# Kernel optimization log

Measured on AMD Instinct MI355X. Metric: run time of the kernel, lower is better.

## Reference

```python
import jax, jax.numpy as jnp
import numpy as np

B, IN, OUT, K = 2048, 1024, 1024, 20


def setup_inputs() -> dict:
    key = jax.random.key(0)
    k1, k2 = jax.random.split(key)
    x = jax.random.normal(k1, (B, IN), dtype=jnp.float32)
    # per-output, per-input spline coefficients: (out_features, in_features, num_knots)
    W = jax.random.normal(k2, (OUT, IN, K), dtype=jnp.float32) * 0.1
    # evenly spaced knot grid on [-2, 2] (linspace)
    knots = jnp.linspace(-2.0, 2.0, K, dtype=jnp.float32)
    return {"x": x, "W": W, "knots": knots}


def reference(x, W, knots):
    # RBF spline basis shared across all output features (this is the fusion
    # the original per-output Python loop misses):
    # basis[b, i, k] = exp(-0.5 * ((x[b, i] - knots[k]) / h)^2)
    h = knots[1] - knots[0]  # uniform knot spacing -> RBF bandwidth
    basis = jnp.exp(-0.5 * jnp.square((x[:, :, None] - knots) / h))  # (B, IN, K)
    # Each SplineLayer o computes sum_{i,k} W[o,i,k] * basis[b,i,k]; the
    # KANBlock concatenates the OUT scalars -> a single einsum.
    return jnp.einsum("bik,oik->bo", basis, W)  # (B, OUT)
```

## Files before the change

### kernel.cpp

```cpp
#include <hip/hip_runtime.h>

#define B_DIM 2048
#define IN_DIM 1024
#define OUT_DIM 1024
#define K_KNOTS 20
#define KR (IN_DIM * K_KNOTS)
#define OUT_ELEMS (B_DIM * OUT_DIM)

#define NB_QUADS (B_DIM * IN_DIM * 5)
#define NB_BASIS_BLK (NB_QUADS / 256)
#define NW4 (OUT_DIM * KR / 8)
#define NB_W_BLK (NW4 / 256)
#define NB_Z_BLK (OUT_ELEMS / (256 * 4))

typedef __bf16 bf16x8 __attribute__((ext_vector_type(8)));
typedef float  f32x4  __attribute__((ext_vector_type(4)));

#define MFMA16(a, b, c) __builtin_amdgcn_mfma_f32_16x16x32_bf16(a, b, c, 0, 0, 0)

__device__ __forceinline__ unsigned short f2bf(float f) {
    unsigned int u = __float_as_uint(f);
    unsigned int r = u + 0x7fffu + ((u >> 16) & 1u);
    return (unsigned short)(r >> 16);
}

__device__ __forceinline__ unsigned int pack2(float lo, float hi) {
    return (unsigned int)f2bf(lo) | ((unsigned int)f2bf(hi) << 16);
}

__device__ __forceinline__ void async_load16(const void* g, void* l) {
    __builtin_amdgcn_global_load_lds(
        (const __attribute__((address_space(1))) void*)g,
        (__attribute__((address_space(3))) void*)l,
        16, 0, 0);
}

__global__ void __launch_bounds__(256) prep_kernel(
        const float* __restrict__ x,
        const float4* __restrict__ Wsrc,
        const float* __restrict__ knots,
        uint2* __restrict__ basis_out,
        uint4* __restrict__ w_out,
        float* __restrict__ out) {
    if (blockIdx.x < NB_BASIS_BLK) {
        unsigned int n = blockIdx.x * 256 + threadIdx.x;
        unsigned int q  = n % 5u;
        unsigned int bi = n / 5u;
        float t0 = knots[0];
        float h  = knots[1] - t0;
        float invh = 1.0f / h;
        float xv = x[bi];
        float k0 = (float)(4 * q);
        float v[4];
#pragma unroll
        for (int j = 0; j < 4; ++j) {
            float t = __builtin_fmaf(k0 + (float)j, h, t0);
            float d = (xv - t) * invh;
            v[j] = __expf(-0.5f * d * d);
        }
        uint2 o;
        o.x = pack2(v[0], v[1]);
        o.y = pack2(v[2], v[3]);
        basis_out[n] = o;
    } else if (blockIdx.x < NB_BASIS_BLK + NB_W_BLK) {
        unsigned int t = (blockIdx.x - NB_BASIS_BLK) * 256 + threadIdx.x;
        float4 a = Wsrc[2 * t];
        float4 b = Wsrc[2 * t + 1];
        uint4 o;
        o.x = pack2(a.x, a.y);
        o.y = pack2(a.z, a.w);
        o.z = pack2(b.x, b.y);
        o.w = pack2(b.z, b.w);
        w_out[t] = o;
    } else {
        unsigned int t = (blockIdx.x - NB_BASIS_BLK - NB_W_BLK) * 256 + threadIdx.x;
        f32x4 z = {0.f, 0.f, 0.f, 0.f};
        *(f32x4*)(out + (size_t)t * 4) = z;
    }
}

#define AOFF(s, h) (((s) * 2 + (h)) * 8192)
#define BOFF(s, h) (32768 + ((s) * 2 + (h)) * 8192)

template <int S>
__device__ __forceinline__ void tile_step(
        int t, int ntiles,
        const unsigned short* __restrict__ Ab,
        const unsigned short* __restrict__ Bb,
        unsigned short* lds,
        f32x4 (&acc)[8][4],
        int m0, int n0, int k0,
        int wave, int wm, int wn, int r15, int c0, int c1,
        int srow8, int scol) {
    const int aB  = S * 16384 + (wm * 128 + r15) * 64;
    const int bB  = 32768 + S * 16384 + (wn * 64 + r15) * 64;
    const int kb1 = k0 + (t + 1) * 64;
    const bool st = (t + 1 < ntiles);

    auto stage = [&](const unsigned short* __restrict__ src, int grow, int kb, int lbase) {
        const unsigned short* g = src + (size_t)(grow + wave * 16 + srow8) * KR + kb + scol;
        async_load16(g,                  &lds[lbase + wave * 1024]);
        async_load16(g + (size_t)8 * KR, &lds[lbase + wave * 1024 + 512]);
    };

    bf16x8 a0[4], a1[4], b0[4], b1[4], s0[4], s1[4];

#pragma unroll
    for (int i = 0; i < 4; ++i) a0[i] = *(const bf16x8*)&lds[aB + i * 1024 + c0];
#pragma unroll
    for (int j = 0; j < 4; ++j) b0[j] = *(const bf16x8*)&lds[bB + j * 1024 + c0];
    __builtin_amdgcn_s_barrier();
    asm volatile("s_waitcnt lgkmcnt(0)" ::: "memory");
    __builtin_amdgcn_sched_barrier(0);
    __builtin_amdgcn_s_setprio(1);
#pragma unroll
    for (int i = 0; i < 4; ++i)
#pragma unroll
        for (int j = 0; j < 4; ++j)
            acc[i][j] = MFMA16(a0[i], b0[j], acc[i][j]);
    __builtin_amdgcn_s_setprio(0);

#pragma unroll
    for (int i = 0; i < 4; ++i) a1[i] = *(const bf16x8*)&lds[aB + i * 1024 + c1];
#pragma unroll
    for (int j = 0; j < 4; ++j) b1[j] = *(const bf16x8*)&lds[bB + j * 1024 + c1];
    __builtin_amdgcn_s_barrier();
    asm volatile("s_waitcnt lgkmcnt(0)" ::: "memory");
    __builtin_amdgcn_sched_barrier(0);
    __builtin_amdgcn_s_setprio(1);
#pragma unroll
    for (int i = 0; i < 4; ++i)
#pragma unroll
        for (int j = 0; j < 4; ++j)
            acc[i][j] = MFMA16(a1[i], b1[j], acc[i][j]);
    __builtin_amdgcn_s_setprio(0);

#pragma unroll
    for (int i = 0; i < 4; ++i) s0[i] = *(const bf16x8*)&lds[aB + (4 + i) * 1024 + c0];
    if (st) {
        stage(Ab, m0,       kb1, AOFF(S ^ 1, 0));
        stage(Ab, m0 + 128, kb1, AOFF(S ^ 1, 1));
    }
    __builtin_amdgcn_s_barrier();
    asm volatile("s_waitcnt lgkmcnt(0)" ::: "memory");
    __builtin_amdgcn_sched_barrier(0);
    __builtin_amdgcn_s_setprio(1);
#pragma unroll
    for (int i = 0; i < 4; ++i)
#pragma unroll
        for (int j = 0; j < 4; ++j)
            acc[4 + i][j] = MFMA16(s0[i], b0[j], acc[4 + i][j]);
    __builtin_amdgcn_s_setprio(0);

#pragma unroll
    for (int i = 0; i < 4; ++i) s1[i] = *(const bf16x8*)&lds[aB + (4 + i) * 1024 + c1];
    if (st) {
        stage(Bb, n0,       kb1, BOFF(S ^ 1, 0));
        stage(Bb, n0 + 128, kb1, BOFF(S ^ 1, 1));
    }
    __builtin_amdgcn_s_barrier();
    asm volatile("s_waitcnt lgkmcnt(0)" ::: "memory");
    __builtin_amdgcn_sched_barrier(0);
    __builtin_amdgcn_s_setprio(1);
#pragma unroll
    for (int i = 0; i < 4; ++i)
#pragma unroll
        for (int j = 0; j < 4; ++j)
            acc[4 + i][j] = MFMA16(s1[i], b1[j], acc[4 + i][j]);
    __builtin_amdgcn_s_setprio(0);

    if (st) asm volatile("s_waitcnt vmcnt(0)" ::: "memory");
    __builtin_amdgcn_s_barrier();
}

template <int KS, bool ATOMIC>
__device__ __forceinline__ void gemm_body(
        const unsigned short* __restrict__ Ab,
        const unsigned short* __restrict__ Bb,
        float* __restrict__ out,
        unsigned short* lds) {
    constexpr int KPBk   = KR / KS;
    constexpr int NTILES = KPBk / 64;

    const int id  = blockIdx.x;
    const int z   = id & 7;
    const int ord = id >> 3;
    const int mt  = ord & 7;
    const int nt  = ord >> 3;
    const int m0  = mt * 256;
    const int n0  = nt * 256;
    const int k0  = z * KPBk;

    const int tid  = threadIdx.x;
    const int wave = tid >> 6;
    const int lane = tid & 63;
    const int wm   = wave >> 2;
    const int wn   = wave & 3;

    const int srow8 = lane >> 3;
    const int scol  = ((lane & 7) ^ srow8) * 8;

    auto stage = [&](const unsigned short* __restrict__ src, int grow, int kb, int lbase) {
        const unsigned short* g = src + (size_t)(grow + wave * 16 + srow8) * KR + kb + scol;
        async_load16(g,                  &lds[lbase + wave * 1024]);
        async_load16(g + (size_t)8 * KR, &lds[lbase + wave * 1024 + 512]);
    };

    f32x4 acc[8][4];
#pragma unroll
    for (int i = 0; i < 8; ++i)
#pragma unroll
        for (int j = 0; j < 4; ++j) acc[i][j] = (f32x4){0.f, 0.f, 0.f, 0.f};

    const int q   = lane >> 4;
    const int r15 = lane & 15;
    const int r7  = lane & 7;
    const int c0  = (q ^ r7) * 8;
    const int c1  = ((4 + q) ^ r7) * 8;

    stage(Ab, m0,       k0, AOFF(0, 0));
    stage(Ab, m0 + 128, k0, AOFF(0, 1));
    stage(Bb, n0,       k0, BOFF(0, 0));
    stage(Bb, n0 + 128, k0, BOFF(0, 1));
    asm volatile("s_waitcnt vmcnt(0)" ::: "memory");
    __builtin_amdgcn_s_barrier();

    for (int tt = 0; tt < NTILES; tt += 2) {
        tile_step<0>(tt,     NTILES, Ab, Bb, lds, acc, m0, n0, k0,
                     wave, wm, wn, r15, c0, c1, srow8, scol);
        tile_step<1>(tt + 1, NTILES, Ab, Bb, lds, acc, m0, n0, k0,
                     wave, wm, wn, r15, c0, c1, srow8, scol);
    }

    float* dst = ATOMIC ? out : out + (size_t)z * OUT_ELEMS;
#pragma unroll
    for (int i = 0; i < 8; ++i)
#pragma unroll
        for (int j = 0; j < 4; ++j)
#pragma unroll
            for (int r = 0; r < 4; ++r) {
                const int row = m0 + wm * 128 + i * 16 + q * 4 + r;
                const int c   = n0 + wn * 64  + j * 16 + r15;
                if (ATOMIC)
                    atomicAdd(&dst[(size_t)row * OUT_DIM + c], acc[i][j][r]);
                else
                    dst[(size_t)row * OUT_DIM + c] = acc[i][j][r];
            }
}

template <int KS, bool ATOMIC>
__global__ void __launch_bounds__(512, 2)
kan_gemm8(const unsigned short* __restrict__ Ab,
          const unsigned short* __restrict__ Bb,
          float* __restrict__ out) {
    __shared__ __align__(16) unsigned short lds[65536];
    gemm_body<KS, ATOMIC>(Ab, Bb, out, lds);
}

template <int KS>
__global__ void kan_reduce(const float* __restrict__ part, float* __restrict__ out) {
    const int idx = (blockIdx.x * 256 + threadIdx.x) * 4;
    f32x4 s = *(const f32x4*)(part + idx);
#pragma unroll
    for (int z = 1; z < KS; ++z)
        s += *(const f32x4*)(part + (size_t)z * OUT_ELEMS + idx);
    *(f32x4*)(out + idx) = s;
}

__global__ void kan_fallback(const float* __restrict__ x,
                             const float* __restrict__ W,
                             const float* __restrict__ knots,
                             float* __restrict__ out) {
    __shared__ float basis[256 * K_KNOTS];
    const int b = blockIdx.x;
    const int o = blockIdx.y * blockDim.x + threadIdx.x;
    const float invh = 1.0f / (knots[1] - knots[0]);
    const float* w = W + (size_t)o * KR;
    float sum = 0.f;
    for (int i0 = 0; i0 < IN_DIM; i0 += 256) {
        __syncthreads();
        for (int idx = threadIdx.x; idx < 256 * K_KNOTS; idx += blockDim.x) {
            const int i = i0 + idx / K_KNOTS;
            const int k = idx % K_KNOTS;
            const float d = (x[(size_t)b * IN_DIM + i] - knots[k]) * invh;
            basis[idx] = __expf(-0.5f * d * d);
        }
        __syncthreads();
        for (int r = 0; r < 256 * K_KNOTS; ++r)
            sum += basis[r] * w[(size_t)i0 * K_KNOTS + r];
    }
    out[(size_t)b * OUT_DIM + o] = sum;
}

extern "C" void kernel_launch(void* const* d_in, const int* in_sizes, int n_in,
                              void* d_out, int out_size, void* d_ws, size_t ws_size,
                              hipStream_t stream) {
    const float* x     = (const float*)d_in[0];
    const float* W     = (const float*)d_in[1];
    const float* knots = (const float*)d_in[2];
    float* out = (float*)d_out;

    const size_t basis_bytes = (size_t)B_DIM * KR * 2;
    const size_t wb_bytes    = (size_t)OUT_DIM * KR * 2;
    const size_t part8_bytes = (size_t)8 * OUT_ELEMS * 4;

    unsigned short* Ab = (unsigned short*)d_ws;
    unsigned short* Bb = (unsigned short*)((char*)d_ws + basis_bytes);
    float* part = (float*)((char*)d_ws + basis_bytes + wb_bytes);

    if (ws_size >= basis_bytes + wb_bytes) {
        prep_kernel<<<dim3(NB_BASIS_BLK + NB_W_BLK + NB_Z_BLK), dim3(256), 0, stream>>>(
            x, (const float4*)W, knots, (uint2*)Ab, (uint4*)Bb, out);
        kan_gemm8<8, true><<<dim3(256), dim3(512), 0, stream>>>(Ab, Bb, out);
        (void)part; (void)part8_bytes;
    } else {
        kan_fallback<<<dim3(B_DIM, OUT_DIM / 256), dim3(256), 0, stream>>>(x, W, knots, out);
    }
}
```

Before: 273.9 us.

## Fuse basis generation and W bf16 conversion into GEMM tile staging

Removes the separate prep kernel that materialised the bf16 basis matrix and bf16 W copy in global memory. Each GEMM block now computes RBF basis values from x and converts fp32 W to bf16 on the fly, writing both into LDS through register stores instead of async global-to-LDS loads. Atomic accumulation is replaced with split-K partial buffers plus a separate reduce kernel. This trades the global round-trip of the intermediates for redundant exp computation (each basis tile is recomputed by every N-tile block), synchronous register-path loads that may expose latency, and extra traffic for the partial sums.

```diff
diff --git a/kernel.cpp b/kernel.cpp
--- a/kernel.cpp
+++ b/kernel.cpp
@@ -6,12 +6,7 @@
 #define K_KNOTS 20
 #define KR (IN_DIM * K_KNOTS)
 #define OUT_ELEMS (B_DIM * OUT_DIM)
-
-#define NB_QUADS (B_DIM * IN_DIM * 5)
-#define NB_BASIS_BLK (NB_QUADS / 256)
-#define NW4 (OUT_DIM * KR / 8)
-#define NB_W_BLK (NW4 / 256)
-#define NB_Z_BLK (OUT_ELEMS / (256 * 4))
+#define KS 8
 
 typedef __bf16 bf16x8 __attribute__((ext_vector_type(8)));
 typedef float  f32x4  __attribute__((ext_vector_type(4)));
@@ -28,80 +23,51 @@
     return (unsigned int)f2bf(lo) | ((unsigned int)f2bf(hi) << 16);
 }
 
-__device__ __forceinline__ void async_load16(const void* g, void* l) {
-    __builtin_amdgcn_global_load_lds(
-        (const __attribute__((address_space(1))) void*)g,
-        (__attribute__((address_space(3))) void*)l,
-        16, 0, 0);
-}
-
-__global__ void __launch_bounds__(256) prep_kernel(
-        const float* __restrict__ x,
-        const float4* __restrict__ Wsrc,
-        const float* __restrict__ knots,
-        uint2* __restrict__ basis_out,
-        uint4* __restrict__ w_out,
-        float* __restrict__ out) {
-    if (blockIdx.x < NB_BASIS_BLK) {
-        unsigned int n = blockIdx.x * 256 + threadIdx.x;
-        unsigned int q  = n % 5u;
-        unsigned int bi = n / 5u;
-        float t0 = knots[0];
-        float h  = knots[1] - t0;
-        float invh = 1.0f / h;
-        float xv = x[bi];
-        float k0 = (float)(4 * q);
-        float v[4];
-#pragma unroll
-        for (int j = 0; j < 4; ++j) {
-            float t = __builtin_fmaf(k0 + (float)j, h, t0);
-            float d = (xv - t) * invh;
-            v[j] = __expf(-0.5f * d * d);
-        }
-        uint2 o;
-        o.x = pack2(v[0], v[1]);
-        o.y = pack2(v[2], v[3]);
-        basis_out[n] = o;
-    } else if (blockIdx.x < NB_BASIS_BLK + NB_W_BLK) {
-        unsigned int t = (blockIdx.x - NB_BASIS_BLK) * 256 + threadIdx.x;
-        float4 a = Wsrc[2 * t];
-        float4 b = Wsrc[2 * t + 1];
-        uint4 o;
-        o.x = pack2(a.x, a.y);
-        o.y = pack2(a.z, a.w);
-        o.z = pack2(b.x, b.y);
-        o.w = pack2(b.z, b.w);
-        w_out[t] = o;
-    } else {
-        unsigned int t = (blockIdx.x - NB_BASIS_BLK - NB_W_BLK) * 256 + threadIdx.x;
-        f32x4 z = {0.f, 0.f, 0.f, 0.f};
-        *(f32x4*)(out + (size_t)t * 4) = z;
-    }
+__device__ __forceinline__ uint4 basis8(const float* __restrict__ x,
+                                        int row, int cb,
+                                        float t0k, float h, float invh) {
+    const int i0  = cb / K_KNOTS;
+    const int kk0 = cb - i0 * K_KNOTS;
+    const int i1  = i0 + (i0 < IN_DIM - 1 ? 1 : 0);
+    const float xv0 = x[(size_t)row * IN_DIM + i0];
+    const float xv1 = x[(size_t)row * IN_DIM + i1];
+    float v[8];
+#pragma unroll
+    for (int j = 0; j < 8; ++j) {
+        const int kk   = kk0 + j;
+        const bool cr  = kk >= K_KNOTS;
+        const float xv = cr ? xv1 : xv0;
+        const float kf = (float)(cr ? kk - K_KNOTS : kk);
+        const float tt = __builtin_fmaf(kf, h, t0k);
+        const float d  = (xv - tt) * invh;
+        v[j] = __expf(-0.5f * d * d);
+    }
+    uint4 o;
+    o.x = pack2(v[0], v[1]); o.y = pack2(v[2], v[3]);
+    o.z = pack2(v[4], v[5]); o.w = pack2(v[6], v[7]);
+    return o;
 }
 
 #define AOFF(s, h) (((s) * 2 + (h)) * 8192)
 #define BOFF(s, h) (32768 + ((s) * 2 + (h)) * 8192)
 
 template <int S>
-__device__ __forceinline__ void tile_step(
+__device__ __forceinline__ void tile_step_f(
         int t, int ntiles,
-        const unsigned short* __restrict__ Ab,
-        const unsigned short* __restrict__ Bb,
+        const float* __restrict__ x,
+        const float* __restrict__ Wf,
         unsigned short* lds,
         f32x4 (&acc)[8][4],
         int m0, int n0, int k0,
-        int wave, int wm, int wn, int r15, int c0, int c1,
-        int srow8, int scol) {
-    const int aB  = S * 16384 + (wm * 128 + r15) * 64;
-    const int bB  = 32768 + S * 16384 + (wn * 64 + r15) * 64;
-    const int kb1 = k0 + (t + 1) * 64;
-    const bool st = (t + 1 < ntiles);
-
-    auto stage = [&](const unsigned short* __restrict__ src, int grow, int kb, int lbase) {
-        const unsigned short* g = src + (size_t)(grow + wave * 16 + srow8) * KR + kb + scol;
-        async_load16(g,                  &lds[lbase + wave * 1024]);
-        async_load16(g + (size_t)8 * KR, &lds[lbase + wave * 1024 + 512]);
-    };
+        int wave, int lane, int wm, int wn, int r15, int c0, int c1,
+        int srow8, int scol,
+        float t0k, float h, float invh) {
+    const int aB   = S * 16384 + (wm * 128 + r15) * 64;
+    const int bB   = 32768 + S * 16384 + (wn * 64 + r15) * 64;
+    const int kb1  = k0 + (t + 1) * 64;
+    const bool st  = (t + 1 < ntiles);
+    const int cbn  = kb1 + scol;
+    const int ldsw = wave * 1024 + lane * 8;
 
     bf16x8 a0[4], a1[4], b0[4], b1[4], s0[4], s1[4];
 
@@ -137,10 +103,6 @@
 
 #pragma unroll
     for (int i = 0; i < 4; ++i) s0[i] = *(const bf16x8*)&lds[aB + (4 + i) * 1024 + c0];
-    if (st) {
-        stage(Ab, m0,       kb1, AOFF(S ^ 1, 0));
-        stage(Ab, m0 + 128, kb1, AOFF(S ^ 1, 1));
-    }
     __builtin_amdgcn_s_barrier();
     asm volatile("s_waitcnt lgkmcnt(0)" ::: "memory");
     __builtin_amdgcn_sched_barrier(0);
@@ -152,12 +114,29 @@
             acc[4 + i][j] = MFMA16(s0[i], b0[j], acc[4 + i][j]);
     __builtin_amdgcn_s_setprio(0);
 
+    f32x4 wA0, wA1, wB0, wB1, wC0, wC1, wD0, wD1;
+    if (st) {
+        const float* g0 = Wf + (size_t)(n0 + wave * 16 + srow8) * KR + cbn;
+        const float* g1 = g0 + (size_t)8 * KR;
+        const float* g2 = g0 + (size_t)128 * KR;
+        const float* g3 = g0 + (size_t)136 * KR;
+        wA0 = *(const f32x4*)g0;       wA1 = *(const f32x4*)(g0 + 4);
+        wB0 = *(const f32x4*)g1;       wB1 = *(const f32x4*)(g1 + 4);
+        wC0 = *(const f32x4*)g2;       wC1 = *(const f32x4*)(g2 + 4);
+        wD0 = *(const f32x4*)g3;       wD1 = *(const f32x4*)(g3 + 4);
+        const int ra = m0 + wave * 16 + srow8;
+        uint4 d0 = basis8(x, ra,       cbn, t0k, h, invh);
+        uint4 d1 = basis8(x, ra + 8,   cbn, t0k, h, invh);
+        uint4 d2 = basis8(x, ra + 128, cbn, t0k, h, invh);
+        uint4 d3 = basis8(x, ra + 136, cbn, t0k, h, invh);
+        *(uint4*)&lds[AOFF(S ^ 1, 0) + ldsw]       = d0;
+        *(uint4*)&lds[AOFF(S ^ 1, 0) + 512 + ldsw] = d1;
+        *(uint4*)&lds[AOFF(S ^ 1, 1) + ldsw]       = d2;
+        *(uint4*)&lds[AOFF(S ^ 1, 1) + 512 + ldsw] = d3;
+    }
+
 #pragma unroll
     for (int i = 0; i < 4; ++i) s1[i] = *(const bf16x8*)&lds[aB + (4 + i) * 1024 + c1];
-    if (st) {
-        stage(Bb, n0,       kb1, BOFF(S ^ 1, 0));
-        stage(Bb, n0 + 128, kb1, BOFF(S ^ 1, 1));
-    }
     __builtin_amdgcn_s_barrier();
     asm volatile("s_waitcnt lgkmcnt(0)" ::: "memory");
     __builtin_amdgcn_sched_barrier(0);
@@ -169,16 +148,32 @@
             acc[4 + i][j] = MFMA16(s1[i], b1[j], acc[4 + i][j]);
     __builtin_amdgcn_s_setprio(0);
 
-    if (st) asm volatile("s_waitcnt vmcnt(0)" ::: "memory");
-    __builtin_amdgcn_s_barrier();
-}
-
-template <int KS, bool ATOMIC>
-__device__ __forceinline__ void gemm_body(
-        const unsigned short* __restrict__ Ab,
-        const unsigned short* __restrict__ Bb,
-        float* __restrict__ out,
-        unsigned short* lds) {
+    if (st) {
+        uint4 o0 = make_uint4(pack2(wA0[0], wA0[1]), pack2(wA0[2], wA0[3]),
+                              pack2(wA1[0], wA1[1]), pack2(wA1[2], wA1[3]));
+        uint4 o1 = make_uint4(pack2(wB0[0], wB0[1]), pack2(wB0[2], wB0[3]),
+                              pack2(wB1[0], wB1[1]), pack2(wB1[2], wB1[3]));
+        uint4 o2 = make_uint4(pack2(wC0[0], wC0[1]), pack2(wC0[2], wC0[3]),
+                              pack2(wC1[0], wC1[1]), pack2(wC1[2], wC1[3]));
+        uint4 o3 = make_uint4(pack2(wD0[0], wD0[1]), pack2(wD0[2], wD0[3]),
+                              pack2(wD1[0], wD1[1]), pack2(wD1[2], wD1[3]));
+        *(uint4*)&lds[BOFF(S ^ 1, 0) + ldsw]       = o0;
+        *(uint4*)&lds[BOFF(S ^ 1, 0) + 512 + ldsw] = o1;
+        *(uint4*)&lds[BOFF(S ^ 1, 1) + ldsw]       = o2;
+        *(uint4*)&lds[BOFF(S ^ 1, 1) + 512 + ldsw] = o3;
+    }
+
+    asm volatile("s_waitcnt lgkmcnt(0)" ::: "memory");
+    __builtin_amdgcn_s_barrier();
+}
+
+__global__ void __launch_bounds__(512, 2)
+kan_gemmf(const float* __restrict__ x,
+          const float* __restrict__ Wf,
+          const float* __restrict__ knots,
+          float* __restrict__ part) {
+    __shared__ __align__(16) unsigned short lds[65536];
+
     constexpr int KPBk   = KR / KS;
     constexpr int NTILES = KPBk / 64;
 
@@ -200,11 +195,9 @@
     const int srow8 = lane >> 3;
     const int scol  = ((lane & 7) ^ srow8) * 8;
 
-    auto stage = [&](const unsigned short* __restrict__ src, int grow, int kb, int lbase) {
-        const unsigned short* g = src + (size_t)(grow + wave * 16 + srow8) * KR + kb + scol;
-        async_load16(g,                  &lds[lbase + wave * 1024]);
-        async_load16(g + (size_t)8 * KR, &lds[lbase + wave * 1024 + 512]);
-    };
+    const float t0k  = knots[0];
+    const float h    = knots[1] - t0k;
+    const float invh = 1.0f / h;
 
     f32x4 acc[8][4];
 #pragma unroll
@@ -218,21 +211,52 @@
     const int c0  = (q ^ r7) * 8;
     const int c1  = ((4 + q) ^ r7) * 8;
 
-    stage(Ab, m0,       k0, AOFF(0, 0));
-    stage(Ab, m0 + 128, k0, AOFF(0, 1));
-    stage(Bb, n0,       k0, BOFF(0, 0));
-    stage(Bb, n0 + 128, k0, BOFF(0, 1));
-    asm volatile("s_waitcnt vmcnt(0)" ::: "memory");
-    __builtin_amdgcn_s_barrier();
+    {
+        const int cb0  = k0 + scol;
+        const int ldsw = wave * 1024 + lane * 8;
+        const int ra   = m0 + wave * 16 + srow8;
+        uint4 d0 = basis8(x, ra,       cb0, t0k, h, invh);
+        uint4 d1 = basis8(x, ra + 8,   cb0, t0k, h, invh);
+        uint4 d2 = basis8(x, ra + 128, cb0, t0k, h, invh);
+        uint4 d3 = basis8(x, ra + 136, cb0, t0k, h, invh);
+        *(uint4*)&lds[AOFF(0, 0) + ldsw]       = d0;
+        *(uint4*)&lds[AOFF(0, 0) + 512 + ldsw] = d1;
+        *(uint4*)&lds[AOFF(0, 1) + ldsw]       = d2;
+        *(uint4*)&lds[AOFF(0, 1) + 512 + ldsw] = d3;
+        const float* g0 = Wf + (size_t)(n0 + wave * 16 + srow8) * KR + cb0;
+        const float* g1 = g0 + (size_t)8 * KR;
+        const float* g2 = g0 + (size_t)128 * KR;
+        const float* g3 = g0 + (size_t)136 * KR;
+        f32x4 wA0 = *(const f32x4*)g0, wA1 = *(const f32x4*)(g0 + 4);
+        f32x4 wB0 = *(const f32x4*)g1, wB1 = *(const f32x4*)(g1 + 4);
+        f32x4 wC0 = *(const f32x4*)g2, wC1 = *(const f32x4*)(g2 + 4);
+        f32x4 wD0 = *(const f32x4*)g3, wD1 = *(const f32x4*)(g3 + 4);
+        uint4 o0 = make_uint4(pack2(wA0[0], wA0[1]), pack2(wA0[2], wA0[3]),
+                              pack2(wA1[0], wA1[1]), pack2(wA1[2], wA1[3]));
+        uint4 o1 = make_uint4(pack2(wB0[0], wB0[1]), pack2(wB0[2], wB0[3]),
+                              pack2(wB1[0], wB1[1]), pack2(wB1[2], wB1[3]));
+        uint4 o2 = make_uint4(pack2(wC0[0], wC0[1]), pack2(wC0[2], wC0[3]),
+                              pack2(wC1[0], wC1[1]), pack2(wC1[2], wC1[3]));
+        uint4 o3 = make_uint4(pack2(wD0[0], wD0[1]), pack2(wD0[2], wD0[3]),
+                              pack2(wD1[0], wD1[1]), pack2(wD1[2], wD1[3]));
+        *(uint4*)&lds[BOFF(0, 0) + ldsw]       = o0;
+        *(uint4*)&lds[BOFF(0, 0) + 512 + ldsw] = o1;
+        *(uint4*)&lds[BOFF(0, 1) + ldsw]       = o2;
+        *(uint4*)&lds[BOFF(0, 1) + 512 + ldsw] = o3;
+        asm volatile("s_waitcnt lgkmcnt(0)" ::: "memory");
+        __builtin_amdgcn_s_barrier();
+    }
 
     for (int tt = 0; tt < NTILES; tt += 2) {
-        tile_step<0>(tt,     NTILES, Ab, Bb, lds, acc, m0, n0, k0,
-                     wave, wm, wn, r15, c0, c1, srow8, scol);
-        tile_step<1>(tt + 1, NTILES, Ab, Bb, lds, acc, m0, n0, k0,
-                     wave, wm, wn, r15, c0, c1, srow8, scol);
-    }
-
-    float* dst = ATOMIC ? out : out + (size_t)z * OUT_ELEMS;
+        tile_step_f<0>(tt,     NTILES, x, Wf, lds, acc, m0, n0, k0,
+                       wave, lane, wm, wn, r15, c0, c1, srow8, scol,
+                       t0k, h, invh);
+        tile_step_f<1>(tt + 1, NTILES, x, Wf, lds, acc, m0, n0, k0,
+                       wave, lane, wm, wn, r15, c0, c1, srow8, scol,
+                       t0k, h, invh);
+    }
+
+    float* dst = part + (size_t)z * OUT_ELEMS;
 #pragma unroll
     for (int i = 0; i < 8; ++i)
 #pragma unroll
@@ -241,28 +265,16 @@
             for (int r = 0; r < 4; ++r) {
                 const int row = m0 + wm * 128 + i * 16 + q * 4 + r;
                 const int c   = n0 + wn * 64  + j * 16 + r15;
-                if (ATOMIC)
-                    atomicAdd(&dst[(size_t)row * OUT_DIM + c], acc[i][j][r]);
-                else
-                    dst[(size_t)row * OUT_DIM + c] = acc[i][j][r];
+                dst[(size_t)row * OUT_DIM + c] = acc[i][j][r];
             }
 }
 
-template <int KS, bool ATOMIC>
-__global__ void __launch_bounds__(512, 2)
-kan_gemm8(const unsigned short* __restrict__ Ab,
-          const unsigned short* __restrict__ Bb,
-          float* __restrict__ out) {
-    __shared__ __align__(16) unsigned short lds[65536];
-    gemm_body<KS, ATOMIC>(Ab, Bb, out, lds);
-}
-
-template <int KS>
+template <int KSr>
 __global__ void kan_reduce(const float* __restrict__ part, float* __restrict__ out) {
     const int idx = (blockIdx.x * 256 + threadIdx.x) * 4;
     f32x4 s = *(const f32x4*)(part + idx);
 #pragma unroll
-    for (int z = 1; z < KS; ++z)
+    for (int z = 1; z < KSr; ++z)
         s += *(const f32x4*)(part + (size_t)z * OUT_ELEMS + idx);
     *(f32x4*)(out + idx) = s;
 }
@@ -300,19 +312,12 @@
     const float* knots = (const float*)d_in[2];
     float* out = (float*)d_out;
 
-    const size_t basis_bytes = (size_t)B_DIM * KR * 2;
-    const size_t wb_bytes    = (size_t)OUT_DIM * KR * 2;
-    const size_t part8_bytes = (size_t)8 * OUT_ELEMS * 4;
-
-    unsigned short* Ab = (unsigned short*)d_ws;
-    unsigned short* Bb = (unsigned short*)((char*)d_ws + basis_bytes);
-    float* part = (float*)((char*)d_ws + basis_bytes + wb_bytes);
-
-    if (ws_size >= basis_bytes + wb_bytes) {
-        prep_kernel<<<dim3(NB_BASIS_BLK + NB_W_BLK + NB_Z_BLK), dim3(256), 0, stream>>>(
-            x, (const float4*)W, knots, (uint2*)Ab, (uint4*)Bb, out);
-        kan_gemm8<8, true><<<dim3(256), dim3(512), 0, stream>>>(Ab, Bb, out);
-        (void)part; (void)part8_bytes;
+    const size_t part_bytes = (size_t)KS * OUT_ELEMS * 4;
+    float* part = (float*)d_ws;
+
+    if (ws_size >= part_bytes) {
+        kan_gemmf<<<dim3(256), dim3(512), 0, stream>>>(x, W, knots, part);
+        kan_reduce<KS><<<dim3(OUT_ELEMS / (256 * 4)), dim3(256), 0, stream>>>(part, out);
     } else {
         kan_fallback<<<dim3(B_DIM, OUT_DIM / 256), dim3(256), 0, stream>>>(x, W, knots, out);
     }
```

New measurement: 282.0 us. +3.0%, slower.

## Replace atomic split-K output with partial buffers plus reduce; widen basis stores

Applied to the files above, without the earlier changes.

The GEMM no longer zeroes the output and atomically adds its eight split-K partials. Each split now writes plain stores into its own partial buffer, and a separate reduce kernel sums the eight slices. The basis prep kernel also computes two quads per thread and writes 16-byte stores, handling the case where a pair spans two inputs. This removes atomic contention and the zeroing pass, but adds 64 MB of partial writes plus reads, one more kernel launch, and a larger workspace requirement.

```diff
diff --git a/kernel.cpp b/kernel.cpp
--- a/kernel.cpp
+++ b/kernel.cpp
@@ -6,12 +6,12 @@
 #define K_KNOTS 20
 #define KR (IN_DIM * K_KNOTS)
 #define OUT_ELEMS (B_DIM * OUT_DIM)
-
-#define NB_QUADS (B_DIM * IN_DIM * 5)
-#define NB_BASIS_BLK (NB_QUADS / 256)
+#define KS 8
+
+#define NPAIRS (B_DIM * IN_DIM * 5 / 2)
+#define NB_BASIS_BLK (NPAIRS / 256)
 #define NW4 (OUT_DIM * KR / 8)
 #define NB_W_BLK (NW4 / 256)
-#define NB_Z_BLK (OUT_ELEMS / (256 * 4))
 
 typedef __bf16 bf16x8 __attribute__((ext_vector_type(8)));
 typedef float  f32x4  __attribute__((ext_vector_type(4)));
@@ -39,30 +39,42 @@
         const float* __restrict__ x,
         const float4* __restrict__ Wsrc,
         const float* __restrict__ knots,
-        uint2* __restrict__ basis_out,
-        uint4* __restrict__ w_out,
-        float* __restrict__ out) {
+        uint4* __restrict__ basis_out,
+        uint4* __restrict__ w_out) {
     if (blockIdx.x < NB_BASIS_BLK) {
-        unsigned int n = blockIdx.x * 256 + threadIdx.x;
-        unsigned int q  = n % 5u;
-        unsigned int bi = n / 5u;
-        float t0 = knots[0];
-        float h  = knots[1] - t0;
-        float invh = 1.0f / h;
-        float xv = x[bi];
-        float k0 = (float)(4 * q);
-        float v[4];
+        const unsigned int p  = blockIdx.x * 256 + threadIdx.x;
+        const unsigned int n0 = 2 * p;
+        const unsigned int q0  = n0 % 5u;
+        const unsigned int bi0 = n0 / 5u;
+        const float t0   = knots[0];
+        const float h    = knots[1] - t0;
+        const float invh = 1.0f / h;
+
+        const bool cross = (q0 == 4u);
+        const unsigned int bi1 = bi0 + (cross ? 1u : 0u);
+        const float xv0 = x[bi0];
+        const float xv1 = x[bi1];
+        const float kA = (float)(4u * q0);
+        const float kB = cross ? 0.f : kA + 4.f;
+
+        float v[8];
 #pragma unroll
         for (int j = 0; j < 4; ++j) {
-            float t = __builtin_fmaf(k0 + (float)j, h, t0);
-            float d = (xv - t) * invh;
+            float t = __builtin_fmaf(kA + (float)j, h, t0);
+            float d = (xv0 - t) * invh;
             v[j] = __expf(-0.5f * d * d);
         }
-        uint2 o;
-        o.x = pack2(v[0], v[1]);
-        o.y = pack2(v[2], v[3]);
-        basis_out[n] = o;
-    } else if (blockIdx.x < NB_BASIS_BLK + NB_W_BLK) {
+#pragma unroll
+        for (int j = 0; j < 4; ++j) {
+            float t = __builtin_fmaf(kB + (float)j, h, t0);
+            float d = (xv1 - t) * invh;
+            v[4 + j] = __expf(-0.5f * d * d);
+        }
+        uint4 o;
+        o.x = pack2(v[0], v[1]); o.y = pack2(v[2], v[3]);
+        o.z = pack2(v[4], v[5]); o.w = pack2(v[6], v[7]);
+        basis_out[p] = o;
+    } else {
         unsigned int t = (blockIdx.x - NB_BASIS_BLK) * 256 + threadIdx.x;
         float4 a = Wsrc[2 * t];
         float4 b = Wsrc[2 * t + 1];
@@ -72,10 +84,6 @@
         o.z = pack2(b.x, b.y);
         o.w = pack2(b.z, b.w);
         w_out[t] = o;
-    } else {
-        unsigned int t = (blockIdx.x - NB_BASIS_BLK - NB_W_BLK) * 256 + threadIdx.x;
-        f32x4 z = {0.f, 0.f, 0.f, 0.f};
-        *(f32x4*)(out + (size_t)t * 4) = z;
     }
 }
 
@@ -173,12 +181,12 @@
     __builtin_amdgcn_s_barrier();
 }
 
-template <int KS, bool ATOMIC>
-__device__ __forceinline__ void gemm_body(
-        const unsigned short* __restrict__ Ab,
-        const unsigned short* __restrict__ Bb,
-        float* __restrict__ out,
-        unsigned short* lds) {
+__global__ void __launch_bounds__(512, 2)
+kan_gemm8(const unsigned short* __restrict__ Ab,
+          const unsigned short* __restrict__ Bb,
+          float* __restrict__ part) {
+    __shared__ __align__(16) unsigned short lds[65536];
+
     constexpr int KPBk   = KR / KS;
     constexpr int NTILES = KPBk / 64;
 
@@ -232,7 +240,7 @@
                      wave, wm, wn, r15, c0, c1, srow8, scol);
     }
 
-    float* dst = ATOMIC ? out : out + (size_t)z * OUT_ELEMS;
+    float* dst = part + (size_t)z * OUT_ELEMS;
 #pragma unroll
     for (int i = 0; i < 8; ++i)
 #pragma unroll
@@ -241,28 +249,16 @@
             for (int r = 0; r < 4; ++r) {
                 const int row = m0 + wm * 128 + i * 16 + q * 4 + r;
                 const int c   = n0 + wn * 64  + j * 16 + r15;
-                if (ATOMIC)
-                    atomicAdd(&dst[(size_t)row * OUT_DIM + c], acc[i][j][r]);
-                else
-                    dst[(size_t)row * OUT_DIM + c] = acc[i][j][r];
+                dst[(size_t)row * OUT_DIM + c] = acc[i][j][r];
             }
 }
 
-template <int KS, bool ATOMIC>
-__global__ void __launch_bounds__(512, 2)
-kan_gemm8(const unsigned short* __restrict__ Ab,
-          const unsigned short* __restrict__ Bb,
-          float* __restrict__ out) {
-    __shared__ __align__(16) unsigned short lds[65536];
-    gemm_body<KS, ATOMIC>(Ab, Bb, out, lds);
-}
-
-template <int KS>
+template <int KSr>
 __global__ void kan_reduce(const float* __restrict__ part, float* __restrict__ out) {
     const int idx = (blockIdx.x * 256 + threadIdx.x) * 4;
     f32x4 s = *(const f32x4*)(part + idx);
 #pragma unroll
-    for (int z = 1; z < KS; ++z)
+    for (int z = 1; z < KSr; ++z)
         s += *(const f32x4*)(part + (size_t)z * OUT_ELEMS + idx);
     *(f32x4*)(out + idx) = s;
 }
@@ -302,17 +298,17 @@
 
     const size_t basis_bytes = (size_t)B_DIM * KR * 2;
     const size_t wb_bytes    = (size_t)OUT_DIM * KR * 2;
-    const size_t part8_bytes = (size_t)8 * OUT_ELEMS * 4;
+    const size_t part_bytes  = (size_t)KS * OUT_ELEMS * 4;
 
     unsigned short* Ab = (unsigned short*)d_ws;
     unsigned short* Bb = (unsigned short*)((char*)d_ws + basis_bytes);
     float* part = (float*)((char*)d_ws + basis_bytes + wb_bytes);
 
-    if (ws_size >= basis_bytes + wb_bytes) {
-        prep_kernel<<<dim3(NB_BASIS_BLK + NB_W_BLK + NB_Z_BLK), dim3(256), 0, stream>>>(
-            x, (const float4*)W, knots, (uint2*)Ab, (uint4*)Bb, out);
-        kan_gemm8<8, true><<<dim3(256), dim3(512), 0, stream>>>(Ab, Bb, out);
-        (void)part; (void)part8_bytes;
+    if (ws_size >= basis_bytes + wb_bytes + part_bytes) {
+        prep_kernel<<<dim3(NB_BASIS_BLK + NB_W_BLK), dim3(256), 0, stream>>>(
+            x, (const float4*)W, knots, (uint4*)Ab, (uint4*)Bb);
+        kan_gemm8<<<dim3(256), dim3(512), 0, stream>>>(Ab, Bb, part);
+        kan_reduce<KS><<<dim3(OUT_ELEMS / (256 * 4)), dim3(256), 0, stream>>>(part, out);
     } else {
         kan_fallback<<<dim3(B_DIM, OUT_DIM / 256), dim3(256), 0, stream>>>(x, W, knots, out);
     }
```

Result: faster. 246.2 us (-10.1%).
